# Kernel optimization log

Hardware: AMD Instinct MI355X
Metric: run time of the kernel (lower is better)

## Reference

```python
import jax, jax.numpy as jnp
import numpy as np

THRESHOLD = 0.9  # module buffer _threshold (starting_threshold)


def setup_inputs() -> dict:
    key = jax.random.key(0)
    k_x, k_w = jax.random.split(key)
    B, T, D = 64, 577, 768
    x = jax.random.normal(k_x, (B, T, D), dtype=jnp.float32)
    # nn.Linear(in_dim, 1): weight [1, D] -> stored as vector [D], bias [1]
    w = jax.random.normal(k_w, (D,), dtype=jnp.float32) * (1.0 / np.sqrt(D))
    b = jnp.zeros((1,), dtype=jnp.float32)
    return {"x": x, "w": w, "b": b}


def reference(x, w, b):
    B, T, D = x.shape
    density = int(T * THRESHOLD)  # static: int(577*0.9) = 519
    # head: Linear(D,1) -> sigmoid -> [B, T]  (dropout is identity in eval)
    prob = jax.nn.sigmoid(jnp.einsum('btd,d->bt', x, w) + b[0])
    # keep top-`density` tokens by score (sorted descending, like torch.topk)
    _, top_idx = jax.lax.top_k(prob, density)
    tokens = jnp.take_along_axis(x, top_idx[..., None], axis=1)  # [B, density, D]
    # bottom (T - density) tokens: topk(largest=False) == topk of -prob,
    # which yields values sorted ascending in prob, matching torch
    n_skip = T - density  # 58 > 0
    neg_vals, skip_idx = jax.lax.top_k(-prob, n_skip)
    skip_tokens = jnp.take_along_axis(x, skip_idx[..., None], axis=1)  # [B, n_skip, D]
    weights = jax.nn.softmax(-neg_vals, axis=-1)  # softmax over skipped probs
    summary_token = jnp.sum(skip_tokens * weights[..., None], axis=1, keepdims=True)  # [B,1,D]
    return tokens, skip_tokens, summary_token
```

## Files before the change

### kernel.cpp

```cpp
#include <hip/hip_runtime.h>
#include <math.h>

#define BB 64
#define TT 577
#define DD 768
#define DENS 519
#define NSKIP 58
#define NROWS (BB * TT)

typedef float vf4 __attribute__((ext_vector_type(4)));

__device__ inline unsigned long long key_of(double z) {
    long long b = __double_as_longlong(z);
    return (b < 0) ? ~(unsigned long long)b
                   : ((unsigned long long)b | 0x8000000000000000ULL);
}
__device__ inline double key_inv(unsigned long long k) {
    long long b = (k >> 63) ? (long long)(k & 0x7fffffffffffffffULL)
                            : ~(long long)k;
    return __longlong_as_double(b);
}

__global__ __launch_bounds__(1024) void k_rank(const float* __restrict__ x,
                                               const float* __restrict__ w,
                                               const float* __restrict__ bias,
                                               int* __restrict__ dstRow,
                                               float* __restrict__ out) {
    __shared__ unsigned long long key[TT];
    __shared__ int   skipIdx[NSKIP];
    __shared__ float wsh[NSKIP];
    const int b    = blockIdx.x;
    const int tid  = threadIdx.x;
    const int wid  = tid >> 6;
    const int lane = tid & 63;
    const float* xb = x + (size_t)b * TT * DD;

    {
        const float4* w4 = (const float4*)w;
        const float4 wv0 = w4[lane];
        const float4 wv1 = w4[lane + 64];
        const float4 wv2 = w4[lane + 128];
        const double bz = (double)bias[0];
        for (int t = wid; t < TT; t += 16) {
            const float4* r4 = (const float4*)(xb + (size_t)t * DD);
            float4 a0 = r4[lane];
            float4 a1 = r4[lane + 64];
            float4 a2 = r4[lane + 128];
            double acc = (double)a0.x * (double)wv0.x + (double)a0.y * (double)wv0.y
                       + (double)a0.z * (double)wv0.z + (double)a0.w * (double)wv0.w;
            acc += (double)a1.x * (double)wv1.x + (double)a1.y * (double)wv1.y
                 + (double)a1.z * (double)wv1.z + (double)a1.w * (double)wv1.w;
            acc += (double)a2.x * (double)wv2.x + (double)a2.y * (double)wv2.y
                 + (double)a2.z * (double)wv2.z + (double)a2.w * (double)wv2.w;
#pragma unroll
            for (int off = 32; off; off >>= 1)
                acc += __shfl_down(acc, off, 64);
            if (lane == 0) key[t] = key_of(acc + bz);
        }
    }
    __syncthreads();

    if (tid < TT) {
        const unsigned long long ki = key[tid];
        int rd = 0;
#pragma unroll 8
        for (int j = 0; j < TT; ++j) {
            unsigned long long kj = key[j];
            rd += ((kj > ki) | ((kj == ki) & (j < tid))) ? 1 : 0;
        }
        int dst;
        if (rd < DENS) {
            dst = b * DENS + rd;
        } else {
            int ra = (TT - 1) - rd;
            dst = BB * DENS + b * NSKIP + ra;
            skipIdx[ra] = tid;
        }
        dstRow[b * TT + tid] = dst;
    }
    __syncthreads();

    if (tid < 64) {
        double pv = -1.0e300;
        if (tid < NSKIP) {
            double z = key_inv(key[skipIdx[tid]]);
            pv = 1.0 / (1.0 + exp(-z));
        }
        double m = pv;
#pragma unroll
        for (int off = 32; off; off >>= 1) {
            double o = __shfl_down(m, off, 64);
            m = (o > m) ? o : m;
        }
        m = __shfl(m, 0, 64);
        double e = (tid < NSKIP) ? exp(pv - m) : 0.0;
        double s = e;
#pragma unroll
        for (int off = 32; off; off >>= 1)
            s += __shfl_down(s, off, 64);
        s = __shfl(s, 0, 64);
        if (tid < NSKIP) wsh[tid] = (float)(e / s);
    }
    __syncthreads();

    if (tid < DD) {
        float acc = 0.f;
#pragma unroll
        for (int k = 0; k < NSKIP; ++k)
            acc += wsh[k] * xb[(size_t)skipIdx[k] * DD + tid];
        out[(size_t)NROWS * DD + (size_t)b * DD + tid] = acc;
    }
}

__global__ __launch_bounds__(256) void k_copy(const float* __restrict__ x,
                                              const int* __restrict__ dstRow,
                                              float* __restrict__ out) {
    int wave = (int)((blockIdx.x * blockDim.x + threadIdx.x) >> 6);
    int lane = threadIdx.x & 63;
    if (wave >= NROWS) return;
    int dst = dstRow[wave];
    const vf4* s4 = (const vf4*)(x + (size_t)wave * DD);
    vf4* d4 = (vf4*)(out + (size_t)dst * DD);
#pragma unroll
    for (int c = 0; c < 3; ++c) {
        vf4 v = s4[lane + 64 * c];
        __builtin_nontemporal_store(v, &d4[lane + 64 * c]);
    }
}

extern "C" void kernel_launch(void* const* d_in, const int* in_sizes, int n_in,
                              void* d_out, int out_size, void* d_ws, size_t ws_size,
                              hipStream_t stream) {
    const float* x    = (const float*)d_in[0];
    const float* w    = (const float*)d_in[1];
    const float* bias = (const float*)d_in[2];
    float* out = (float*)d_out;
    int* dstRow = (int*)d_ws;

    k_rank<<<BB, 1024, 0, stream>>>(x, w, bias, dstRow, out);
    k_copy<<<NROWS / 4, 256, 0, stream>>>(x, dstRow, out);
}
```

Baseline: 247.9 us.

## Split score computation into a separate grid-wide kernel before ranking

Moves the per-token dot product out of the 64-block rank kernel into its own kernel with one wave per row across all B*T rows. The scores are written as sortable keys to workspace, and the rank kernel then only loads them. This spreads the 113 MB read of x over the whole GPU instead of 64 workgroups, which were likely bandwidth-starved. It costs an extra launch and a small keys round trip through memory.

```diff
diff --git a/kernel.cpp b/kernel.cpp
--- a/kernel.cpp
+++ b/kernel.cpp
@@ -21,43 +21,41 @@
     return __longlong_as_double(b);
 }
 
-__global__ __launch_bounds__(1024) void k_rank(const float* __restrict__ x,
-                                               const float* __restrict__ w,
-                                               const float* __restrict__ bias,
-                                               int* __restrict__ dstRow,
-                                               float* __restrict__ out) {
+__global__ __launch_bounds__(256) void k_prob(const float* __restrict__ x,
+                                              const float* __restrict__ w,
+                                              const float* __restrict__ bias,
+                                              unsigned long long* __restrict__ keys) {
+    int wave = (int)((blockIdx.x * blockDim.x + threadIdx.x) >> 6);
+    int lane = threadIdx.x & 63;
+    if (wave >= NROWS) return;
+    const float4* r4 = (const float4*)(x + (size_t)wave * DD);
+    const float4* w4 = (const float4*)w;
+    double acc = 0.0;
+#pragma unroll
+    for (int i = 0; i < 3; ++i) {
+        float4 a = r4[lane + 64 * i];
+        float4 b = w4[lane + 64 * i];
+        acc += (double)a.x * (double)b.x + (double)a.y * (double)b.y
+             + (double)a.z * (double)b.z + (double)a.w * (double)b.w;
+    }
+#pragma unroll
+    for (int off = 32; off; off >>= 1)
+        acc += __shfl_down(acc, off, 64);
+    if (lane == 0) keys[wave] = key_of(acc + (double)bias[0]);
+}
+
+__global__ __launch_bounds__(1024) void k_map(const float* __restrict__ x,
+                                              const unsigned long long* __restrict__ keysG,
+                                              int* __restrict__ dstRow,
+                                              float* __restrict__ out) {
     __shared__ unsigned long long key[TT];
     __shared__ int   skipIdx[NSKIP];
     __shared__ float wsh[NSKIP];
-    const int b    = blockIdx.x;
-    const int tid  = threadIdx.x;
-    const int wid  = tid >> 6;
-    const int lane = tid & 63;
+    const int b   = blockIdx.x;
+    const int tid = threadIdx.x;
     const float* xb = x + (size_t)b * TT * DD;
 
-    {
-        const float4* w4 = (const float4*)w;
-        const float4 wv0 = w4[lane];
-        const float4 wv1 = w4[lane + 64];
-        const float4 wv2 = w4[lane + 128];
-        const double bz = (double)bias[0];
-        for (int t = wid; t < TT; t += 16) {
-            const float4* r4 = (const float4*)(xb + (size_t)t * DD);
-            float4 a0 = r4[lane];
-            float4 a1 = r4[lane + 64];
-            float4 a2 = r4[lane + 128];
-            double acc = (double)a0.x * (double)wv0.x + (double)a0.y * (double)wv0.y
-                       + (double)a0.z * (double)wv0.z + (double)a0.w * (double)wv0.w;
-            acc += (double)a1.x * (double)wv1.x + (double)a1.y * (double)wv1.y
-                 + (double)a1.z * (double)wv1.z + (double)a1.w * (double)wv1.w;
-            acc += (double)a2.x * (double)wv2.x + (double)a2.y * (double)wv2.y
-                 + (double)a2.z * (double)wv2.z + (double)a2.w * (double)wv2.w;
-#pragma unroll
-            for (int off = 32; off; off >>= 1)
-                acc += __shfl_down(acc, off, 64);
-            if (lane == 0) key[t] = key_of(acc + bz);
-        }
-    }
+    if (tid < TT) key[tid] = keysG[b * TT + tid];
     __syncthreads();
 
     if (tid < TT) {
@@ -135,8 +133,12 @@
     const float* w    = (const float*)d_in[1];
     const float* bias = (const float*)d_in[2];
     float* out = (float*)d_out;
-    int* dstRow = (int*)d_ws;
+    char* ws = (char*)d_ws;
 
-    k_rank<<<BB, 1024, 0, stream>>>(x, w, bias, dstRow, out);
+    unsigned long long* keys = (unsigned long long*)ws;
+    int* dstRow = (int*)(ws + 295424);
+
+    k_prob<<<NROWS / 4, 256, 0, stream>>>(x, w, bias, keys);
+    k_map<<<BB, 1024, 0, stream>>>(x, keys, dstRow, out);
     k_copy<<<NROWS / 4, 256, 0, stream>>>(x, dstRow, out);
 }
```

Result: faster. 235.4 us (-5.0%).
